# Kernel tuning notes

Measured on AMD Instinct MI355X. Metric: run time of the kernel, lower is better.

Reference implementation:

```python
import jax, jax.numpy as jnp
import numpy as np

N = 50000      # nodes
E = 800000     # edges (before self loops)
HID = 128      # hidden_dim
FEAT = 128     # feat_dim
NEG_SLOPE = 0.2
BN_EPS = 1e-5


def setup_inputs() -> dict:
    key = jax.random.key(0)
    ks = jax.random.split(key, 16)
    s = lambda d: 1.0 / np.sqrt(d).astype(np.float32)
    return {
        "x": jax.random.normal(ks[0], (N, HID), jnp.float32),
        "edge_index": jax.random.randint(ks[1], (2, E), 0, N, jnp.int32),
        # GATConv 1 (hidden -> hidden)
        "W1": jax.random.normal(ks[2], (HID, HID), jnp.float32) * s(HID),
        "att_src1": jax.random.normal(ks[3], (HID,), jnp.float32) * s(HID),
        "att_dst1": jax.random.normal(ks[4], (HID,), jnp.float32) * s(HID),
        "b1": jnp.zeros((HID,), jnp.float32),
        # BatchNorm1d(hidden) -- eval mode buffers/params
        "bn_gamma": jnp.ones((HID,), jnp.float32),
        "bn_beta": jnp.zeros((HID,), jnp.float32),
        "bn_mean": jax.random.normal(ks[5], (HID,), jnp.float32) * 0.1,
        "bn_var": jax.random.uniform(ks[6], (HID,), jnp.float32, 0.5, 1.5),
        # GATConv 2 (hidden -> feat)
        "W2": jax.random.normal(ks[7], (HID, FEAT), jnp.float32) * s(HID),
        "att_src2": jax.random.normal(ks[8], (FEAT,), jnp.float32) * s(FEAT),
        "att_dst2": jax.random.normal(ks[9], (FEAT,), jnp.float32) * s(FEAT),
        "b2": jnp.zeros((FEAT,), jnp.float32),
    }


def _gat_conv(x, W, att_src, att_dst, bias, src, dst, n_nodes):
    """PyG GATConv, heads=1: gather -> edge attn -> segment softmax -> scatter."""
    h = x @ W                                   # [N, d_out]
    a_s = h @ att_src                           # [N]
    a_d = h @ att_dst                           # [N]
    e = jax.nn.leaky_relu(a_s[src] + a_d[dst], NEG_SLOPE)  # [E']
    # numerically-stable softmax over incoming edges of each dst node
    e_max = jax.ops.segment_max(e, dst, num_segments=n_nodes)
    ex = jnp.exp(e - e_max[dst])
    denom = jax.ops.segment_sum(ex, dst, num_segments=n_nodes)
    alpha = ex / (denom[dst] + 1e-16)           # [E']
    out = jax.ops.segment_sum(alpha[:, None] * h[src], dst, num_segments=n_nodes)
    return out + bias


def reference(x, edge_index, W1, att_src1, att_dst1, b1,
              bn_gamma, bn_beta, bn_mean, bn_var,
              W2, att_src2, att_dst2, b2):
    n = x.shape[0]
    loops = jnp.arange(n, dtype=edge_index.dtype)
    src = jnp.concatenate([edge_index[0], loops])
    dst = jnp.concatenate([edge_index[1], loops])

    h = jax.nn.relu(_gat_conv(x, W1, att_src1, att_dst1, b1, src, dst, n))
    # BatchNorm1d in eval mode (running stats); dropout is identity in eval
    h = (h - bn_mean) * jax.lax.rsqrt(bn_var + BN_EPS) * bn_gamma + bn_beta
    out = jax.nn.relu(_gat_conv(h, W2, att_src2, att_dst2, b2, src, dst, n))
    return out
```

## Files before the change

kernel.cpp:

```cpp
#include <hip/hip_runtime.h>

typedef unsigned short u16;
typedef unsigned int   u32;
typedef __attribute__((ext_vector_type(8))) short bh8;
typedef __attribute__((ext_vector_type(4))) float fx4;

__device__ __forceinline__ float b2f(u16 h){ return __uint_as_float(((u32)h) << 16); }
__device__ __forceinline__ u16   f2b(float f){
  u32 u = __float_as_uint(f);
  u32 r = u + 0x7FFFu + ((u >> 16) & 1u);
  return (u16)(r >> 16);
}
__device__ __forceinline__ float lo16(u32 w){ return b2f((u16)(w & 0xFFFFu)); }
__device__ __forceinline__ float hi16(u32 w){ return b2f((u16)(w >> 16)); }

__global__ void r17_zero(int* p, int n){
  int t = blockIdx.x*blockDim.x + threadIdx.x;
  if (t < n) p[t] = 0;
}

__global__ void r17_hist_prep(const int* __restrict__ ei, int E, int Ep, int* cnt,
                              u16* __restrict__ rank,
                              const float* __restrict__ W1, const float* __restrict__ as1,
                              const float* __restrict__ ad1,
                              const float* __restrict__ W2, const float* __restrict__ as2,
                              const float* __restrict__ ad2,
                              u16* __restrict__ w1H, u16* __restrict__ w1L,
                              u16* __restrict__ w2H, u16* __restrict__ w2L,
                              float* __restrict__ ws1, float* __restrict__ wd1,
                              float* __restrict__ ws2, float* __restrict__ wd2){
  int b = blockIdx.x;
  int t = threadIdx.x;
  if (b < 16){
    const float* W = (b < 8) ? W1 : W2;
    u16* HT = (b < 8) ? w1H : w2H;
    u16* LT = (b < 8) ? w1L : w2L;
    int n0 = (b & 7) * 16;
    #pragma unroll
    for (int it = 0; it < 8; ++it){
      int idx = it*256 + t;
      int n = n0 + (idx >> 7);
      int k = idx & 127;
      float w = W[(size_t)k*128 + n];
      u16 h = f2b(w);
      HT[(size_t)n*128 + k] = h;
      LT[(size_t)n*128 + k] = f2b(w - b2f(h));
    }
    return;
  }
  if (b == 16){
    int which = t >> 6;
    const float* W   = (which < 2) ? W1 : W2;
    const float* att = (which == 0) ? as1 : (which == 1) ? ad1 : (which == 2) ? as2 : ad2;
    float* outv      = (which == 0) ? ws1 : (which == 1) ? wd1 : (which == 2) ? ws2 : wd2;
    int k0 = (t & 63) * 2;
    #pragma unroll
    for (int kk = 0; kk < 2; ++kk){
      int k = k0 + kk;
      float s = 0.f;
      for (int c = 0; c < 128; ++c) s = fmaf(W[(size_t)k*128 + c], att[c], s);
      outv[k] = s;
    }
    return;
  }
  int g = (b - 17)*256 + t;
  if (g >= Ep) return;
  int dst = (g < E) ? ei[E + g] : (g - E);
  int r = atomicAdd(&cnt[dst], 1);
  rank[g] = (u16)r;
}

__global__ void r17_scan1(const int* in, int n, int* incl, int* bsums){
  __shared__ int tmp[256];
  int t = threadIdx.x; int g = blockIdx.x*256 + t;
  int v = (g < n) ? in[g] : 0;
  tmp[t] = v; __syncthreads();
  for (int off = 1; off < 256; off <<= 1){
    int u = (t >= off) ? tmp[t - off] : 0;
    __syncthreads();
    tmp[t] += u;
    __syncthreads();
  }
  if (g < n) incl[g] = tmp[t];
  if (t == 255) bsums[blockIdx.x] = tmp[255];
}

__global__ void r17_scan2(int* bsums, int nb){
  __shared__ int tmp[256];
  int t = threadIdx.x;
  int v = (t < nb) ? bsums[t] : 0;
  tmp[t] = v; __syncthreads();
  for (int off = 1; off < 256; off <<= 1){
    int u = (t >= off) ? tmp[t - off] : 0;
    __syncthreads();
    tmp[t] += u;
    __syncthreads();
  }
  if (t < nb) bsums[t] = tmp[t];
}

__global__ void r17_scan3(const int* incl, const int* cnt, const int* bsums,
                          int n, int* offs){
  int t = threadIdx.x; int b = blockIdx.x; int g = b*256 + t;
  if (g >= n) return;
  int add = (b > 0) ? bsums[b-1] : 0;
  offs[g] = incl[g] - cnt[g] + add;
}

__device__ __forceinline__ void gemm16_wave(
    const float* __restrict__ X, const u16* __restrict__ wH, const u16* __restrict__ wL,
    const float* __restrict__ wsv, const float* __restrict__ wdv,
    u16* __restrict__ HB, float* __restrict__ AS, float* __restrict__ AD,
    int nrows, int w, int lane)
{
  int r0 = w * 16;
  if (r0 >= nrows) return;
  int rloc = lane & 15;
  int q    = lane >> 4;
  int myrow = r0 + rloc;
  bool act = (myrow < nrows);
  int rsafe = act ? myrow : (nrows - 1);

  fx4 acc[8] = {};
  float ds = 0.f, dd = 0.f;

  const u16* wHrow = wH + (size_t)rloc * 128;
  const u16* wLrow = wL + (size_t)rloc * 128;

  #pragma unroll
  for (int kk = 0; kk < 4; ++kk){
    int kbase = kk*32 + q*8;
    const float* xp = X + (size_t)rsafe*128 + kbase;
    float4 xa = *(const float4*)xp;
    float4 xb = *(const float4*)(xp + 4);
    float xv[8] = {xa.x, xa.y, xa.z, xa.w, xb.x, xb.y, xb.z, xb.w};
    if (!act){
      #pragma unroll
      for (int i = 0; i < 8; ++i) xv[i] = 0.f;
    }
    const float* sp = wsv + kbase;
    const float* dp = wdv + kbase;
    bh8 xh, xl;
    #pragma unroll
    for (int i = 0; i < 8; ++i){
      ds = fmaf(xv[i], sp[i], ds);
      dd = fmaf(xv[i], dp[i], dd);
      u16 h = f2b(xv[i]);
      xh[i] = (short)h;
      xl[i] = (short)f2b(xv[i] - b2f(h));
    }
    #pragma unroll
    for (int cf = 0; cf < 8; ++cf){
      bh8 wh = *(const bh8*)(wHrow + (size_t)cf*2048 + kbase);
      bh8 wl = *(const bh8*)(wLrow + (size_t)cf*2048 + kbase);
      acc[cf] = __builtin_amdgcn_mfma_f32_16x16x32_bf16(wh, xh, acc[cf], 0, 0, 0);
      acc[cf] = __builtin_amdgcn_mfma_f32_16x16x32_bf16(wl, xh, acc[cf], 0, 0, 0);
      acc[cf] = __builtin_amdgcn_mfma_f32_16x16x32_bf16(wh, xl, acc[cf], 0, 0, 0);
    }
  }
  ds += __shfl_xor(ds, 16); ds += __shfl_xor(ds, 32);
  dd += __shfl_xor(dd, 16); dd += __shfl_xor(dd, 32);
  if (act && q == 0){ AS[myrow] = ds; AD[myrow] = dd; }
  if (act){
    u16* hrow = HB + (size_t)myrow*128 + q*4;
    #pragma unroll
    for (int cf = 0; cf < 8; ++cf){
      uint2 pb;
      pb.x = (u32)f2b(acc[cf][0]) | ((u32)f2b(acc[cf][1]) << 16);
      pb.y = (u32)f2b(acc[cf][2]) | ((u32)f2b(acc[cf][3]) << 16);
      *(uint2*)(hrow + cf*16) = pb;
    }
  }
}

__global__ __launch_bounds__(256)
void r17_gemm_fill(const float* __restrict__ X,
                   const u16* __restrict__ wH, const u16* __restrict__ wL,
                   const float* __restrict__ wsv, const float* __restrict__ wdv,
                   u16* __restrict__ HB, float* __restrict__ AS, float* __restrict__ AD,
                   int nrows, int gemmBlocks,
                   const int* __restrict__ ei, int E, int Ep,
                   const int* __restrict__ offs, const u16* __restrict__ rank,
                   u16* __restrict__ csr){
  int t = threadIdx.x;
  if ((int)blockIdx.x >= gemmBlocks){
    int g = ((int)blockIdx.x - gemmBlocks)*256 + t;
    if (g < Ep){
      int src, dst;
      if (g < E){ src = ei[g]; dst = ei[E + g]; } else { src = g - E; dst = g - E; }
      int pos = offs[dst] + (int)rank[g];
      csr[pos] = (u16)src;
    }
    return;
  }
  int w = (int)blockIdx.x*4 + (t >> 6);
  gemm16_wave(X, wH, wL, wsv, wdv, HB, AS, AD, nrows, w, t & 63);
}

__global__ __launch_bounds__(256)
void r17_gemm(const float* __restrict__ X,
              const u16* __restrict__ wH, const u16* __restrict__ wL,
              const float* __restrict__ wsv, const float* __restrict__ wdv,
              u16* __restrict__ HB, float* __restrict__ AS, float* __restrict__ AD,
              int nrows){
  int w = (int)blockIdx.x*4 + (threadIdx.x >> 6);
  gemm16_wave(X, wH, wL, wsv, wdv, HB, AS, AD, nrows, w, threadIdx.x & 63);
}

__global__ __launch_bounds__(256)
void r17_aggregate(const u16* __restrict__ HB, const float* __restrict__ AS,
                   const float* __restrict__ AD,
                   const int* __restrict__ offs, const u16* __restrict__ csr,
                   const float* __restrict__ bias,
                   const float* __restrict__ gamma_, const float* __restrict__ beta_,
                   const float* __restrict__ mean_, const float* __restrict__ var_,
                   float* __restrict__ outp, int n, int doBN){
  int wid  = (blockIdx.x*256 + threadIdx.x) >> 6;
  int lane = threadIdx.x & 63;
  if (wid >= n) return;
  int beg = offs[wid], end = offs[wid+1];
  int deg = end - beg;
  float ad = AD[wid];
  int c2 = lane*2;
  float a0 = 0.f, a1 = 0.f;

  if (deg <= 64){
    int   my_s = 0;
    float my_e = -3.0e38f;
    int myk = beg + lane;
    bool act = (myk < end);
    if (act){
      my_s = (int)csr[myk];
      float e = AS[my_s] + ad;
      my_e = (e > 0.f) ? e : 0.2f*e;
    }
    float m = my_e;
    #pragma unroll
    for (int off = 32; off >= 1; off >>= 1) m = fmaxf(m, __shfl_xor(m, off));
    float pz = act ? __expf(my_e - m) : 0.f;
    float den = pz;
    #pragma unroll
    for (int off = 32; off >= 1; off >>= 1) den += __shfl_xor(den, off);
    float my_al = pz / (den + 1e-16f);

    int j = 0;
    for (; j + 8 <= deg; j += 8){
      int   s0 = __shfl(my_s, j),   s1 = __shfl(my_s, j+1);
      int   s2 = __shfl(my_s, j+2), s3 = __shfl(my_s, j+3);
      int   s4 = __shfl(my_s, j+4), s5 = __shfl(my_s, j+5);
      int   s6 = __shfl(my_s, j+6), s7 = __shfl(my_s, j+7);
      float l0 = __shfl(my_al, j),   l1 = __shfl(my_al, j+1);
      float l2 = __shfl(my_al, j+2), l3 = __shfl(my_al, j+3);
      float l4 = __shfl(my_al, j+4), l5 = __shfl(my_al, j+5);
      float l6 = __shfl(my_al, j+6), l7 = __shfl(my_al, j+7);
      u32 h0 = *(const u32*)&HB[(size_t)s0*128 + c2];
      u32 h1 = *(const u32*)&HB[(size_t)s1*128 + c2];
      u32 h2 = *(const u32*)&HB[(size_t)s2*128 + c2];
      u32 h3 = *(const u32*)&HB[(size_t)s3*128 + c2];
      u32 h4 = *(const u32*)&HB[(size_t)s4*128 + c2];
      u32 h5 = *(const u32*)&HB[(size_t)s5*128 + c2];
      u32 h6 = *(const u32*)&HB[(size_t)s6*128 + c2];
      u32 h7 = *(const u32*)&HB[(size_t)s7*128 + c2];
      a0 = fmaf(l0, lo16(h0), a0); a1 = fmaf(l0, hi16(h0), a1);
      a0 = fmaf(l1, lo16(h1), a0); a1 = fmaf(l1, hi16(h1), a1);
      a0 = fmaf(l2, lo16(h2), a0); a1 = fmaf(l2, hi16(h2), a1);
      a0 = fmaf(l3, lo16(h3), a0); a1 = fmaf(l3, hi16(h3), a1);
      a0 = fmaf(l4, lo16(h4), a0); a1 = fmaf(l4, hi16(h4), a1);
      a0 = fmaf(l5, lo16(h5), a0); a1 = fmaf(l5, hi16(h5), a1);
      a0 = fmaf(l6, lo16(h6), a0); a1 = fmaf(l6, hi16(h6), a1);
      a0 = fmaf(l7, lo16(h7), a0); a1 = fmaf(l7, hi16(h7), a1);
    }
    for (; j + 4 <= deg; j += 4){
      int   s0 = __shfl(my_s, j),   s1 = __shfl(my_s, j+1);
      int   s2 = __shfl(my_s, j+2), s3 = __shfl(my_s, j+3);
      float l0 = __shfl(my_al, j),   l1 = __shfl(my_al, j+1);
      float l2 = __shfl(my_al, j+2), l3 = __shfl(my_al, j+3);
      u32 h0 = *(const u32*)&HB[(size_t)s0*128 + c2];
      u32 h1 = *(const u32*)&HB[(size_t)s1*128 + c2];
      u32 h2 = *(const u32*)&HB[(size_t)s2*128 + c2];
      u32 h3 = *(const u32*)&HB[(size_t)s3*128 + c2];
      a0 = fmaf(l0, lo16(h0), a0); a1 = fmaf(l0, hi16(h0), a1);
      a0 = fmaf(l1, lo16(h1), a0); a1 = fmaf(l1, hi16(h1), a1);
      a0 = fmaf(l2, lo16(h2), a0); a1 = fmaf(l2, hi16(h2), a1);
      a0 = fmaf(l3, lo16(h3), a0); a1 = fmaf(l3, hi16(h3), a1);
    }
    for (; j < deg; ++j){
      int   s = __shfl(my_s, j);
      float l = __shfl(my_al, j);
      u32 hv = *(const u32*)&HB[(size_t)s*128 + c2];
      a0 = fmaf(l, lo16(hv), a0); a1 = fmaf(l, hi16(hv), a1);
    }
  } else {
    float m = -3.0e38f;
    for (int k = beg + lane; k < end; k += 64){
      int s = (int)csr[k];
      float e = AS[s] + ad; e = (e > 0.f) ? e : 0.2f*e;
      m = fmaxf(m, e);
    }
    #pragma unroll
    for (int off = 32; off >= 1; off >>= 1) m = fmaxf(m, __shfl_xor(m, off));
    float den = 0.f;
    for (int k = beg + lane; k < end; k += 64){
      int s = (int)csr[k];
      float e = AS[s] + ad; e = (e > 0.f) ? e : 0.2f*e;
      den += __expf(e - m);
    }
    #pragma unroll
    for (int off = 32; off >= 1; off >>= 1) den += __shfl_xor(den, off);
    float inv = 1.0f / (den + 1e-16f);
    for (int k = beg; k < end; ++k){
      int s = (int)csr[k];
      float e = AS[s] + ad; e = (e > 0.f) ? e : 0.2f*e;
      float al = __expf(e - m) * inv;
      u32 hv = *(const u32*)&HB[(size_t)s*128 + c2];
      a0 = fmaf(al, lo16(hv), a0); a1 = fmaf(al, hi16(hv), a1);
    }
  }

  float v0 = a0 + bias[c2];
  float v1 = a1 + bias[c2+1];
  v0 = fmaxf(v0, 0.f); v1 = fmaxf(v1, 0.f);
  if (doBN){
    float s0 = gamma_[c2]   * rsqrtf(var_[c2]   + 1e-5f);
    float s1 = gamma_[c2+1] * rsqrtf(var_[c2+1] + 1e-5f);
    v0 = (v0 - mean_[c2])*s0   + beta_[c2];
    v1 = (v1 - mean_[c2+1])*s1 + beta_[c2+1];
  }
  float2 o = {v0, v1};
  ((float2*)(outp + (size_t)wid*128))[lane] = o;
}

extern "C" void kernel_launch(void* const* d_in, const int* in_sizes, int n_in,
                              void* d_out, int out_size, void* d_ws, size_t ws_size,
                              hipStream_t stream){
  const float* x   = (const float*)d_in[0];
  const int*   ei  = (const int*)  d_in[1];
  const float* W1  = (const float*)d_in[2];
  const float* as1 = (const float*)d_in[3];
  const float* ad1 = (const float*)d_in[4];
  const float* b1  = (const float*)d_in[5];
  const float* bng = (const float*)d_in[6];
  const float* bnb = (const float*)d_in[7];
  const float* bnm = (const float*)d_in[8];
  const float* bnv = (const float*)d_in[9];
  const float* W2  = (const float*)d_in[10];
  const float* as2 = (const float*)d_in[11];
  const float* ad2 = (const float*)d_in[12];
  const float* b2  = (const float*)d_in[13];
  float* out = (float*)d_out;

  int N  = in_sizes[0] / 128;
  int E  = in_sizes[1] / 2;
  int Ep = E + N;
  if (N <= 0 || E <= 0) return;

  char* base = (char*)d_ws;
  size_t off = 0;
  auto alloc = [&](size_t bytes)->char*{
    off = (off + 255) & ~(size_t)255;
    char* q = base + off; off += bytes; return q;
  };
  float* AS     = (float*)alloc((size_t)N*4);
  float* AD     = (float*)alloc((size_t)N*4);
  int*   cnt    = (int*)  alloc((size_t)(N+1)*4);
  int*   offs   = (int*)  alloc((size_t)(N+1)*4);
  int*   bsums  = (int*)  alloc(1024);
  u16*   rank   = (u16*)  alloc((size_t)Ep*2);
  u16*   csr    = (u16*)  alloc((size_t)Ep*2);
  u16*   hb     = (u16*)  alloc((size_t)N*128*2);
  float* x2     = (float*)alloc((size_t)N*128*4);
  u16*   w1H    = (u16*)  alloc(128*128*2);
  u16*   w1L    = (u16*)  alloc(128*128*2);
  u16*   w2H    = (u16*)  alloc(128*128*2);
  u16*   w2L    = (u16*)  alloc(128*128*2);
  float* ws1    = (float*)alloc(128*4);
  float* wd1    = (float*)alloc(128*4);
  float* ws2    = (float*)alloc(128*4);
  float* wd2    = (float*)alloc(128*4);

  int n1 = N + 1;
  int zb = (n1 + 255)/256;
  int eb = (Ep + 255)/256;
  int sb = (n1 + 255)/256;
  int nW = (N + 15)/16;
  int gwb = (nW + 3)/4;
  int wb = (N + 3)/4;

  r17_zero     <<<zb, 256, 0, stream>>>(cnt, n1);
  r17_hist_prep<<<eb + 17, 256, 0, stream>>>(ei, E, Ep, cnt, rank,
                                             W1, as1, ad1, W2, as2, ad2,
                                             w1H, w1L, w2H, w2L,
                                             ws1, wd1, ws2, wd2);
  r17_scan1<<<sb, 256, 0, stream>>>(cnt, n1, offs, bsums);
  r17_scan2<<<1, 256, 0, stream>>>(bsums, sb);
  r17_scan3<<<sb, 256, 0, stream>>>(offs, cnt, bsums, n1, offs);

  r17_gemm_fill<<<gwb + eb, 256, 0, stream>>>(x, w1H, w1L, ws1, wd1,
                                              hb, AS, AD, N, gwb,
                                              ei, E, Ep, offs, rank, csr);
  r17_aggregate<<<wb, 256, 0, stream>>>(hb, AS, AD, offs, csr, b1, bng, bnb, bnm, bnv,
                                        x2, N, 1);
  r17_gemm     <<<gwb, 256, 0, stream>>>(x2, w2H, w2L, ws2, wd2, hb, AS, AD, N);
  r17_aggregate<<<wb, 256, 0, stream>>>(hb, AS, AD, offs, csr, b2, 0, 0, 0, 0,
                                        out, N, 0);
}
```

Measured before the change: 301.3 us.

## Split aggregate wave into two edge halves, merge scans, batch edge threads

The aggregate kernel now splits each 64-lane wave into two half-waves. Each half handles alternate edges and loads 4 bf16 channels per lane with 8-byte loads, and the halves are combined by a cross-half shuffle before a float4 store. This doubles memory-level parallelism per edge and halves the edge loop trip count, at the cost of idle lanes in the epilogue. The three-kernel scan is replaced by a single 1024-thread block that does sequential per-thread chunks, removing two launches, but it runs serially on one CU. Histogram and CSR-fill threads now process 4 edges each.

```diff
diff --git a/kernel.cpp b/kernel.cpp
--- a/kernel.cpp
+++ b/kernel.cpp
@@ -14,12 +14,12 @@
 __device__ __forceinline__ float lo16(u32 w){ return b2f((u16)(w & 0xFFFFu)); }
 __device__ __forceinline__ float hi16(u32 w){ return b2f((u16)(w >> 16)); }
 
-__global__ void r17_zero(int* p, int n){
+__global__ void r19_zero(int* p, int n){
   int t = blockIdx.x*blockDim.x + threadIdx.x;
   if (t < n) p[t] = 0;
 }
 
-__global__ void r17_hist_prep(const int* __restrict__ ei, int E, int Ep, int* cnt,
+__global__ void r19_hist_prep(const int* __restrict__ ei, int E, int Ep, int* cnt,
                               u16* __restrict__ rank,
                               const float* __restrict__ W1, const float* __restrict__ as1,
                               const float* __restrict__ ad1,
@@ -39,12 +39,12 @@
     #pragma unroll
     for (int it = 0; it < 8; ++it){
       int idx = it*256 + t;
-      int n = n0 + (idx >> 7);
+      int nn = n0 + (idx >> 7);
       int k = idx & 127;
-      float w = W[(size_t)k*128 + n];
+      float w = W[(size_t)k*128 + nn];
       u16 h = f2b(w);
-      HT[(size_t)n*128 + k] = h;
-      LT[(size_t)n*128 + k] = f2b(w - b2f(h));
+      HT[(size_t)nn*128 + k] = h;
+      LT[(size_t)nn*128 + k] = f2b(w - b2f(h));
     }
     return;
   }
@@ -63,48 +63,36 @@
     }
     return;
   }
-  int g = (b - 17)*256 + t;
-  if (g >= Ep) return;
-  int dst = (g < E) ? ei[E + g] : (g - E);
-  int r = atomicAdd(&cnt[dst], 1);
-  rank[g] = (u16)r;
-}
-
-__global__ void r17_scan1(const int* in, int n, int* incl, int* bsums){
-  __shared__ int tmp[256];
-  int t = threadIdx.x; int g = blockIdx.x*256 + t;
-  int v = (g < n) ? in[g] : 0;
-  tmp[t] = v; __syncthreads();
-  for (int off = 1; off < 256; off <<= 1){
+  int g0 = (b - 17)*1024 + t;
+  #pragma unroll
+  for (int i = 0; i < 4; ++i){
+    int g = g0 + i*256;
+    if (g < Ep){
+      int dst = (g < E) ? ei[E + g] : (g - E);
+      int r = atomicAdd(&cnt[dst], 1);
+      rank[g] = (u16)r;
+    }
+  }
+}
+
+__global__ __launch_bounds__(1024)
+void r19_scan(const int* __restrict__ cnt, int n, int* __restrict__ offs){
+  __shared__ int tmp[1024];
+  int t = threadIdx.x;
+  int chunk = (n + 1023) >> 10;
+  int lo = t*chunk;
+  int hi = lo + chunk; if (hi > n) hi = n;
+  int s = 0;
+  for (int i = lo; i < hi; ++i) s += cnt[i];
+  tmp[t] = s; __syncthreads();
+  for (int off = 1; off < 1024; off <<= 1){
     int u = (t >= off) ? tmp[t - off] : 0;
     __syncthreads();
     tmp[t] += u;
     __syncthreads();
   }
-  if (g < n) incl[g] = tmp[t];
-  if (t == 255) bsums[blockIdx.x] = tmp[255];
-}
-
-__global__ void r17_scan2(int* bsums, int nb){
-  __shared__ int tmp[256];
-  int t = threadIdx.x;
-  int v = (t < nb) ? bsums[t] : 0;
-  tmp[t] = v; __syncthreads();
-  for (int off = 1; off < 256; off <<= 1){
-    int u = (t >= off) ? tmp[t - off] : 0;
-    __syncthreads();
-    tmp[t] += u;
-    __syncthreads();
-  }
-  if (t < nb) bsums[t] = tmp[t];
-}
-
-__global__ void r17_scan3(const int* incl, const int* cnt, const int* bsums,
-                          int n, int* offs){
-  int t = threadIdx.x; int b = blockIdx.x; int g = b*256 + t;
-  if (g >= n) return;
-  int add = (b > 0) ? bsums[b-1] : 0;
-  offs[g] = incl[g] - cnt[g] + add;
+  int run = (t > 0) ? tmp[t-1] : 0;
+  for (int i = lo; i < hi; ++i){ offs[i] = run; run += cnt[i]; }
 }
 
 __device__ __forceinline__ void gemm16_wave(
@@ -174,7 +162,7 @@
 }
 
 __global__ __launch_bounds__(256)
-void r17_gemm_fill(const float* __restrict__ X,
+void r19_gemm_fill(const float* __restrict__ X,
                    const u16* __restrict__ wH, const u16* __restrict__ wL,
                    const float* __restrict__ wsv, const float* __restrict__ wdv,
                    u16* __restrict__ HB, float* __restrict__ AS, float* __restrict__ AD,
@@ -184,12 +172,15 @@
                    u16* __restrict__ csr){
   int t = threadIdx.x;
   if ((int)blockIdx.x >= gemmBlocks){
-    int g = ((int)blockIdx.x - gemmBlocks)*256 + t;
-    if (g < Ep){
-      int src, dst;
-      if (g < E){ src = ei[g]; dst = ei[E + g]; } else { src = g - E; dst = g - E; }
-      int pos = offs[dst] + (int)rank[g];
-      csr[pos] = (u16)src;
+    int g0 = ((int)blockIdx.x - gemmBlocks)*1024 + t;
+    #pragma unroll
+    for (int i = 0; i < 4; ++i){
+      int g = g0 + i*256;
+      if (g < Ep){
+        int src, dst;
+        if (g < E){ src = ei[g]; dst = ei[E + g]; } else { src = g - E; dst = g - E; }
+        csr[offs[dst] + (int)rank[g]] = (u16)src;
+      }
     }
     return;
   }
@@ -198,7 +189,7 @@
 }
 
 __global__ __launch_bounds__(256)
-void r17_gemm(const float* __restrict__ X,
+void r19_gemm(const float* __restrict__ X,
               const u16* __restrict__ wH, const u16* __restrict__ wL,
               const float* __restrict__ wsv, const float* __restrict__ wdv,
               u16* __restrict__ HB, float* __restrict__ AS, float* __restrict__ AD,
@@ -208,7 +199,7 @@
 }
 
 __global__ __launch_bounds__(256)
-void r17_aggregate(const u16* __restrict__ HB, const float* __restrict__ AS,
+void r19_aggregate(const u16* __restrict__ HB, const float* __restrict__ AS,
                    const float* __restrict__ AD,
                    const int* __restrict__ offs, const u16* __restrict__ csr,
                    const float* __restrict__ bias,
@@ -221,16 +212,16 @@
   int beg = offs[wid], end = offs[wid+1];
   int deg = end - beg;
   float ad = AD[wid];
-  int c2 = lane*2;
-  float a0 = 0.f, a1 = 0.f;
+  int h  = lane >> 5;
+  int c4 = (lane & 31) * 4;
+  float a0 = 0.f, a1 = 0.f, a2 = 0.f, a3 = 0.f;
 
   if (deg <= 64){
     int   my_s = 0;
     float my_e = -3.0e38f;
-    int myk = beg + lane;
-    bool act = (myk < end);
+    bool act = (lane < deg);
     if (act){
-      my_s = (int)csr[myk];
+      my_s = (int)csr[beg + lane];
       float e = AS[my_s] + ad;
       my_e = (e > 0.f) ? e : 0.2f*e;
     }
@@ -243,52 +234,34 @@
     for (int off = 32; off >= 1; off >>= 1) den += __shfl_xor(den, off);
     float my_al = pz / (den + 1e-16f);
 
-    int j = 0;
-    for (; j + 8 <= deg; j += 8){
-      int   s0 = __shfl(my_s, j),   s1 = __shfl(my_s, j+1);
-      int   s2 = __shfl(my_s, j+2), s3 = __shfl(my_s, j+3);
-      int   s4 = __shfl(my_s, j+4), s5 = __shfl(my_s, j+5);
-      int   s6 = __shfl(my_s, j+6), s7 = __shfl(my_s, j+7);
-      float l0 = __shfl(my_al, j),   l1 = __shfl(my_al, j+1);
-      float l2 = __shfl(my_al, j+2), l3 = __shfl(my_al, j+3);
-      float l4 = __shfl(my_al, j+4), l5 = __shfl(my_al, j+5);
-      float l6 = __shfl(my_al, j+6), l7 = __shfl(my_al, j+7);
-      u32 h0 = *(const u32*)&HB[(size_t)s0*128 + c2];
-      u32 h1 = *(const u32*)&HB[(size_t)s1*128 + c2];
-      u32 h2 = *(const u32*)&HB[(size_t)s2*128 + c2];
-      u32 h3 = *(const u32*)&HB[(size_t)s3*128 + c2];
-      u32 h4 = *(const u32*)&HB[(size_t)s4*128 + c2];
-      u32 h5 = *(const u32*)&HB[(size_t)s5*128 + c2];
-      u32 h6 = *(const u32*)&HB[(size_t)s6*128 + c2];
-      u32 h7 = *(const u32*)&HB[(size_t)s7*128 + c2];
-      a0 = fmaf(l0, lo16(h0), a0); a1 = fmaf(l0, hi16(h0), a1);
-      a0 = fmaf(l1, lo16(h1), a0); a1 = fmaf(l1, hi16(h1), a1);
-      a0 = fmaf(l2, lo16(h2), a0); a1 = fmaf(l2, hi16(h2), a1);
-      a0 = fmaf(l3, lo16(h3), a0); a1 = fmaf(l3, hi16(h3), a1);
-      a0 = fmaf(l4, lo16(h4), a0); a1 = fmaf(l4, hi16(h4), a1);
-      a0 = fmaf(l5, lo16(h5), a0); a1 = fmaf(l5, hi16(h5), a1);
-      a0 = fmaf(l6, lo16(h6), a0); a1 = fmaf(l6, hi16(h6), a1);
-      a0 = fmaf(l7, lo16(h7), a0); a1 = fmaf(l7, hi16(h7), a1);
-    }
-    for (; j + 4 <= deg; j += 4){
-      int   s0 = __shfl(my_s, j),   s1 = __shfl(my_s, j+1);
-      int   s2 = __shfl(my_s, j+2), s3 = __shfl(my_s, j+3);
-      float l0 = __shfl(my_al, j),   l1 = __shfl(my_al, j+1);
-      float l2 = __shfl(my_al, j+2), l3 = __shfl(my_al, j+3);
-      u32 h0 = *(const u32*)&HB[(size_t)s0*128 + c2];
-      u32 h1 = *(const u32*)&HB[(size_t)s1*128 + c2];
-      u32 h2 = *(const u32*)&HB[(size_t)s2*128 + c2];
-      u32 h3 = *(const u32*)&HB[(size_t)s3*128 + c2];
-      a0 = fmaf(l0, lo16(h0), a0); a1 = fmaf(l0, hi16(h0), a1);
-      a0 = fmaf(l1, lo16(h1), a0); a1 = fmaf(l1, hi16(h1), a1);
-      a0 = fmaf(l2, lo16(h2), a0); a1 = fmaf(l2, hi16(h2), a1);
-      a0 = fmaf(l3, lo16(h3), a0); a1 = fmaf(l3, hi16(h3), a1);
-    }
-    for (; j < deg; ++j){
+    int npair = (deg + 1) >> 1;
+    int k = 0;
+    for (; k + 4 <= npair; k += 4){
+      int j0 = 2*k + h, j1 = j0 + 2, j2 = j0 + 4, j3 = j0 + 6;
+      int   s0 = __shfl(my_s, j0),  s1 = __shfl(my_s, j1);
+      int   s2 = __shfl(my_s, j2),  s3 = __shfl(my_s, j3);
+      float l0 = __shfl(my_al, j0), l1 = __shfl(my_al, j1);
+      float l2 = __shfl(my_al, j2), l3 = __shfl(my_al, j3);
+      uint2 q0 = *(const uint2*)&HB[(size_t)s0*128 + c4];
+      uint2 q1 = *(const uint2*)&HB[(size_t)s1*128 + c4];
+      uint2 q2 = *(const uint2*)&HB[(size_t)s2*128 + c4];
+      uint2 q3 = *(const uint2*)&HB[(size_t)s3*128 + c4];
+      a0 = fmaf(l0, lo16(q0.x), a0); a1 = fmaf(l0, hi16(q0.x), a1);
+      a2 = fmaf(l0, lo16(q0.y), a2); a3 = fmaf(l0, hi16(q0.y), a3);
+      a0 = fmaf(l1, lo16(q1.x), a0); a1 = fmaf(l1, hi16(q1.x), a1);
+      a2 = fmaf(l1, lo16(q1.y), a2); a3 = fmaf(l1, hi16(q1.y), a3);
+      a0 = fmaf(l2, lo16(q2.x), a0); a1 = fmaf(l2, hi16(q2.x), a1);
+      a2 = fmaf(l2, lo16(q2.y), a2); a3 = fmaf(l2, hi16(q2.y), a3);
+      a0 = fmaf(l3, lo16(q3.x), a0); a1 = fmaf(l3, hi16(q3.x), a1);
+      a2 = fmaf(l3, lo16(q3.y), a2); a3 = fmaf(l3, hi16(q3.y), a3);
+    }
+    for (; k < npair; ++k){
+      int j = 2*k + h;
       int   s = __shfl(my_s, j);
       float l = __shfl(my_al, j);
-      u32 hv = *(const u32*)&HB[(size_t)s*128 + c2];
-      a0 = fmaf(l, lo16(hv), a0); a1 = fmaf(l, hi16(hv), a1);
+      uint2 q = *(const uint2*)&HB[(size_t)s*128 + c4];
+      a0 = fmaf(l, lo16(q.x), a0); a1 = fmaf(l, hi16(q.x), a1);
+      a2 = fmaf(l, lo16(q.y), a2); a3 = fmaf(l, hi16(q.y), a3);
     }
   } else {
     float m = -3.0e38f;
@@ -308,26 +281,37 @@
     #pragma unroll
     for (int off = 32; off >= 1; off >>= 1) den += __shfl_xor(den, off);
     float inv = 1.0f / (den + 1e-16f);
-    for (int k = beg; k < end; ++k){
-      int s = (int)csr[k];
+    for (int j = h; j < deg; j += 2){
+      int s = (int)csr[beg + j];
       float e = AS[s] + ad; e = (e > 0.f) ? e : 0.2f*e;
       float al = __expf(e - m) * inv;
-      u32 hv = *(const u32*)&HB[(size_t)s*128 + c2];
-      a0 = fmaf(al, lo16(hv), a0); a1 = fmaf(al, hi16(hv), a1);
-    }
-  }
-
-  float v0 = a0 + bias[c2];
-  float v1 = a1 + bias[c2+1];
-  v0 = fmaxf(v0, 0.f); v1 = fmaxf(v1, 0.f);
-  if (doBN){
-    float s0 = gamma_[c2]   * rsqrtf(var_[c2]   + 1e-5f);
-    float s1 = gamma_[c2+1] * rsqrtf(var_[c2+1] + 1e-5f);
-    v0 = (v0 - mean_[c2])*s0   + beta_[c2];
-    v1 = (v1 - mean_[c2+1])*s1 + beta_[c2+1];
-  }
-  float2 o = {v0, v1};
-  ((float2*)(outp + (size_t)wid*128))[lane] = o;
+      uint2 q = *(const uint2*)&HB[(size_t)s*128 + c4];
+      a0 = fmaf(al, lo16(q.x), a0); a1 = fmaf(al, hi16(q.x), a1);
+      a2 = fmaf(al, lo16(q.y), a2); a3 = fmaf(al, hi16(q.y), a3);
+    }
+  }
+
+  a0 += __shfl_xor(a0, 32); a1 += __shfl_xor(a1, 32);
+  a2 += __shfl_xor(a2, 32); a3 += __shfl_xor(a3, 32);
+  if (lane < 32){
+    float4 bv = *(const float4*)(bias + c4);
+    float v0 = fmaxf(a0 + bv.x, 0.f);
+    float v1 = fmaxf(a1 + bv.y, 0.f);
+    float v2 = fmaxf(a2 + bv.z, 0.f);
+    float v3 = fmaxf(a3 + bv.w, 0.f);
+    if (doBN){
+      float4 gv = *(const float4*)(gamma_ + c4);
+      float4 vv = *(const float4*)(var_   + c4);
+      float4 mv = *(const float4*)(mean_  + c4);
+      float4 be = *(const float4*)(beta_  + c4);
+      v0 = (v0 - mv.x) * (gv.x * rsqrtf(vv.x + 1e-5f)) + be.x;
+      v1 = (v1 - mv.y) * (gv.y * rsqrtf(vv.y + 1e-5f)) + be.y;
+      v2 = (v2 - mv.z) * (gv.z * rsqrtf(vv.z + 1e-5f)) + be.z;
+      v3 = (v3 - mv.w) * (gv.w * rsqrtf(vv.w + 1e-5f)) + be.w;
+    }
+    float4 o = {v0, v1, v2, v3};
+    *(float4*)(outp + (size_t)wid*128 + c4) = o;
+  }
 }
 
 extern "C" void kernel_launch(void* const* d_in, const int* in_sizes, int n_in,
@@ -364,7 +348,6 @@
   float* AD     = (float*)alloc((size_t)N*4);
   int*   cnt    = (int*)  alloc((size_t)(N+1)*4);
   int*   offs   = (int*)  alloc((size_t)(N+1)*4);
-  int*   bsums  = (int*)  alloc(1024);
   u16*   rank   = (u16*)  alloc((size_t)Ep*2);
   u16*   csr    = (u16*)  alloc((size_t)Ep*2);
   u16*   hb     = (u16*)  alloc((size_t)N*128*2);
@@ -378,29 +361,25 @@
   float* ws2    = (float*)alloc(128*4);
   float* wd2    = (float*)alloc(128*4);
 
-  int n1 = N + 1;
-  int zb = (n1 + 255)/256;
-  int eb = (Ep + 255)/256;
-  int sb = (n1 + 255)/256;
-  int nW = (N + 15)/16;
+  int n1  = N + 1;
+  int zb  = (n1 + 255)/256;
+  int ebH = (Ep + 1023)/1024;
+  int nW  = (N + 15)/16;
   int gwb = (nW + 3)/4;
-  int wb = (N + 3)/4;
-
-  r17_zero     <<<zb, 256, 0, stream>>>(cnt, n1);
-  r17_hist_prep<<<eb + 17, 256, 0, stream>>>(ei, E, Ep, cnt, rank,
-                                             W1, as1, ad1, W2, as2, ad2,
-                                             w1H, w1L, w2H, w2L,
-                                             ws1, wd1, ws2, wd2);
-  r17_scan1<<<sb, 256, 0, stream>>>(cnt, n1, offs, bsums);
-  r17_scan2<<<1, 256, 0, stream>>>(bsums, sb);
-  r17_scan3<<<sb, 256, 0, stream>>>(offs, cnt, bsums, n1, offs);
-
-  r17_gemm_fill<<<gwb + eb, 256, 0, stream>>>(x, w1H, w1L, ws1, wd1,
-                                              hb, AS, AD, N, gwb,
-                                              ei, E, Ep, offs, rank, csr);
-  r17_aggregate<<<wb, 256, 0, stream>>>(hb, AS, AD, offs, csr, b1, bng, bnb, bnm, bnv,
+  int wb  = (N + 3)/4;
+
+  r19_zero     <<<zb, 256, 0, stream>>>(cnt, n1);
+  r19_hist_prep<<<ebH + 17, 256, 0, stream>>>(ei, E, Ep, cnt, rank,
+                                              W1, as1, ad1, W2, as2, ad2,
+                                              w1H, w1L, w2H, w2L,
+                                              ws1, wd1, ws2, wd2);
+  r19_scan     <<<1, 1024, 0, stream>>>(cnt, n1, offs);
+  r19_gemm_fill<<<gwb + ebH, 256, 0, stream>>>(x, w1H, w1L, ws1, wd1,
+                                               hb, AS, AD, N, gwb,
+                                               ei, E, Ep, offs, rank, csr);
+  r19_aggregate<<<wb, 256, 0, stream>>>(hb, AS, AD, offs, csr, b1, bng, bnb, bnm, bnv,
                                         x2, N, 1);
-  r17_gemm     <<<gwb, 256, 0, stream>>>(x2, w2H, w2L, ws2, wd2, hb, AS, AD, N);
-  r17_aggregate<<<wb, 256, 0, stream>>>(hb, AS, AD, offs, csr, b2, 0, 0, 0, 0,
+  r19_gemm     <<<gwb, 256, 0, stream>>>(x2, w2H, w2L, ws2, wd2, hb, AS, AD, N);
+  r19_aggregate<<<wb, 256, 0, stream>>>(hb, AS, AD, offs, csr, b2, 0, 0, 0, 0,
                                         out, N, 0);
 }
```

After: 374.0 us. +24.1%, slower.
